# Kernel optimization log

Measured on AMD Instinct MI355X. Metric: run time of the kernel, lower is better.

The kernel has to match this reference:

```python
import jax, jax.numpy as jnp
import numpy as np

N_NODES = 50000
N_EDGES = 600000
D = 128
HIDDEN = 128
OUT = 1


def setup_inputs() -> dict:
    key = jax.random.key(0)
    ks = jax.random.split(key, 6)
    z = jax.random.normal(ks[0], (N_NODES, D), dtype=jnp.float32)
    e = jax.random.randint(ks[1], (2, N_EDGES), 0, N_NODES, dtype=jnp.int64)
    # Linear weights in [in, out] layout; scaled like torch default init
    W1 = jax.random.normal(ks[2], (2 * D, HIDDEN), dtype=jnp.float32) / np.sqrt(2 * D)
    b1 = jax.random.normal(ks[3], (HIDDEN,), dtype=jnp.float32) / np.sqrt(2 * D)
    W2 = jax.random.normal(ks[4], (HIDDEN, OUT), dtype=jnp.float32) / np.sqrt(HIDDEN)
    b2 = jax.random.normal(ks[5], (OUT,), dtype=jnp.float32) / np.sqrt(HIDDEN)
    return {"z": z, "e": e, "W1": W1, "b1": b1, "W2": W2, "b2": b2}


def reference(z, e, W1, b1, W2, b2):
    x_i = z[e[0]]                      # [E, D] gather source nodes
    x_j = z[e[1]]                      # [E, D] gather target nodes
    x = jnp.concatenate([x_i, x_j], axis=1)  # [E, 2D]
    h = jax.nn.relu(x @ W1 + b1)       # [E, HIDDEN]
    out = h @ W2 + b2                  # [E, OUT]
    return jax.nn.sigmoid(out).squeeze()  # [E]
```

## Files before the change

kernel.cpp:

```cpp
#include <hip/hip_runtime.h>


#define DD 128

typedef __attribute__((ext_vector_type(8))) short short8;
typedef __attribute__((ext_vector_type(4))) float floatx4;

static __device__ __forceinline__ unsigned short f2bf(float f) {
  unsigned int u = __builtin_bit_cast(unsigned int, f);
  u += 0x7fffu + ((u >> 16) & 1u);
  return (unsigned short)(u >> 16);
}
static __device__ __forceinline__ float bf2f(unsigned short u) {
  return __builtin_bit_cast(float, (unsigned int)u << 16);
}

__global__ __launch_bounds__(256) void wt_build(
    const float* __restrict__ W1, unsigned short* __restrict__ Wt) {
  const int g = blockIdx.x * 256 + threadIdx.x;
  const int c = g >> 5;
  const int kq = (g & 31) * 4;
  const float* src = (c < 128) ? (W1 + c) : (W1 + 128 * 128 + (c - 128));
  ushort4 o;
  o.x = f2bf(src[(size_t)(kq + 0) * 128]);
  o.y = f2bf(src[(size_t)(kq + 1) * 128]);
  o.z = f2bf(src[(size_t)(kq + 2) * 128]);
  o.w = f2bf(src[(size_t)(kq + 3) * 128]);
  *(ushort4*)&Wt[c * 128 + kq] = o;
}

__global__ __launch_bounds__(512, 4) void node_mfma(
    const float* __restrict__ z, const unsigned short* __restrict__ Wt,
    const float* __restrict__ b1, signed char* __restrict__ gqi,
    signed char* __restrict__ gqj, float* __restrict__ sci,
    float* __restrict__ scj, int n_nodes) {
  __shared__ __align__(16) unsigned short zb[64 * 136];
  const int tid = threadIdx.x;
  const int nb = blockIdx.x * 64;

#pragma unroll
  for (int i = 0; i < 4; ++i) {
    int q = tid + i * 512;
    int nl = q >> 5;
    int node = nb + nl; if (node >= n_nodes) node = n_nodes - 1;
    float4 v = ((const float4*)z)[(size_t)node * 32 + (q & 31)];
    ushort4 o;
    o.x = f2bf(v.x); o.y = f2bf(v.y); o.z = f2bf(v.z); o.w = f2bf(v.w);
    *(ushort4*)&zb[nl * 136 + (q & 31) * 4] = o;
  }

  const int w = tid >> 6, lane = tid & 63;
  const int l15 = lane & 15, quad = lane >> 4;

  short8 a[2][4];
#pragma unroll
  for (int tt = 0; tt < 2; ++tt) {
    const unsigned short* wrow =
        Wt + (size_t)((w * 2 + tt) * 16 + l15) * 128 + quad * 8;
#pragma unroll
    for (int s = 0; s < 4; ++s) a[tt][s] = *(const short8*)(wrow + s * 32);
  }

  floatx4 acc[2][4];
#pragma unroll
  for (int tt = 0; tt < 2; ++tt) {
    floatx4 bias = {0.f, 0.f, 0.f, 0.f};
    if (w < 4) {
      float4 b4 = *(const float4*)&b1[(w * 2 + tt) * 16 + quad * 4];
      bias[0] = b4.x; bias[1] = b4.y; bias[2] = b4.z; bias[3] = b4.w;
    }
#pragma unroll
    for (int nt = 0; nt < 4; ++nt) acc[tt][nt] = bias;
  }

  __syncthreads();

#pragma unroll
  for (int nt = 0; nt < 4; ++nt) {
    short8 bz[4];
#pragma unroll
    for (int s = 0; s < 4; ++s)
      bz[s] = *(const short8*)&zb[(nt * 16 + l15) * 136 + s * 32 + quad * 8];
#pragma unroll
    for (int tt = 0; tt < 2; ++tt)
#pragma unroll
      for (int s = 0; s < 4; ++s)
        acc[tt][nt] = __builtin_amdgcn_mfma_f32_16x16x32_bf16(
            a[tt][s], bz[s], acc[tt][nt], 0, 0, 0);
  }

  __syncthreads();
#pragma unroll
  for (int half = 0; half < 2; ++half) {
    if ((w >> 2) == half) {
      const int cbase = (w & 3) * 32;
#pragma unroll
      for (int nt = 0; nt < 4; ++nt) {
        const int row = (nt * 16 + l15) * 136;
#pragma unroll
        for (int tt = 0; tt < 2; ++tt) {
          const int c = cbase + tt * 16 + quad * 4;
          ushort4 o;
          o.x = f2bf(acc[tt][nt][0]); o.y = f2bf(acc[tt][nt][1]);
          o.z = f2bf(acc[tt][nt][2]); o.w = f2bf(acc[tt][nt][3]);
          *(ushort4*)&zb[row + c] = o;
        }
      }
    }
    __syncthreads();
    {
      const int nl = tid >> 3, p8 = tid & 7;
      const int node = nb + nl;
      const unsigned short* rowp = &zb[nl * 136 + p8 * 16];
      ushort4 u0 = *(const ushort4*)(rowp);
      ushort4 u1 = *(const ushort4*)(rowp + 4);
      ushort4 u2 = *(const ushort4*)(rowp + 8);
      ushort4 u3 = *(const ushort4*)(rowp + 12);
      float f[16];
      f[0] = bf2f(u0.x); f[1] = bf2f(u0.y); f[2] = bf2f(u0.z); f[3] = bf2f(u0.w);
      f[4] = bf2f(u1.x); f[5] = bf2f(u1.y); f[6] = bf2f(u1.z); f[7] = bf2f(u1.w);
      f[8] = bf2f(u2.x); f[9] = bf2f(u2.y); f[10] = bf2f(u2.z); f[11] = bf2f(u2.w);
      f[12] = bf2f(u3.x); f[13] = bf2f(u3.y); f[14] = bf2f(u3.z); f[15] = bf2f(u3.w);
      float am = 0.f;
#pragma unroll
      for (int k = 0; k < 16; ++k) am = fmaxf(am, fabsf(f[k]));
      am = fmaxf(am, __shfl_xor(am, 1));
      am = fmaxf(am, __shfl_xor(am, 2));
      am = fmaxf(am, __shfl_xor(am, 4));
      const float inv = (am > 0.f) ? 127.f / am : 0.f;
      unsigned int wd[4];
#pragma unroll
      for (int k2 = 0; k2 < 4; ++k2) {
        unsigned int v = 0;
#pragma unroll
        for (int b = 0; b < 4; ++b) {
          const int q = (int)rintf(f[k2 * 4 + b] * inv);
          v |= ((unsigned int)(q & 0xff)) << (8 * b);
        }
        wd[k2] = v;
      }
      if (node < n_nodes) {
        signed char* dq = half ? gqj : gqi;
        uint4 pk; pk.x = wd[0]; pk.y = wd[1]; pk.z = wd[2]; pk.w = wd[3];
        ((uint4*)(dq + (size_t)node * 128))[p8] = pk;
        if (p8 == 0) (half ? scj : sci)[node] = am * (1.f / 127.f);
      }
    }
    __syncthreads();
  }
}

__global__ __launch_bounds__(256) void edge_mlp_q(
    const int* __restrict__ e, const signed char* __restrict__ gqi,
    const signed char* __restrict__ gqj, const float* __restrict__ sci,
    const float* __restrict__ scj, const float* __restrict__ W2,
    const float* __restrict__ b2, float* __restrict__ out, int E) {
  const int p = threadIdx.x & 7;
  const float4* wv = (const float4*)W2;
  float4 W[4];
#pragma unroll
  for (int k = 0; k < 4; ++k) W[k] = wv[p * 4 + k];
  const float bias2 = b2[0];

  const int stride = gridDim.x * 32;
  for (int edge = blockIdx.x * 32 + (threadIdx.x >> 3); edge < E; edge += stride) {
    const int i = e[edge];
    const int j = e[E + edge];
    const float si = sci[i];
    const float sj = scj[j];
    const uint4 qa = ((const uint4*)(gqi + (size_t)i * 128))[p];
    const uint4 qb = ((const uint4*)(gqj + (size_t)j * 128))[p];
    const unsigned int ua[4] = {qa.x, qa.y, qa.z, qa.w};
    const unsigned int ub[4] = {qb.x, qb.y, qb.z, qb.w};
    float acc = 0.f;
#pragma unroll
    for (int k = 0; k < 4; ++k) {
      const float wk[4] = {W[k].x, W[k].y, W[k].z, W[k].w};
#pragma unroll
      for (int b = 0; b < 4; ++b) {
        const float af = (float)(int)(signed char)(ua[k] >> (8 * b));
        const float bf = (float)(int)(signed char)(ub[k] >> (8 * b));
        const float h = fmaf(si, af, sj * bf);
        acc = fmaf(fmaxf(h, 0.f), wk[b], acc);
      }
    }
    acc += __shfl_xor(acc, 1);
    acc += __shfl_xor(acc, 2);
    acc += __shfl_xor(acc, 4);
    if (p == 0) {
      out[edge] = 1.f / (1.f + __expf(-(acc + bias2)));
    }
  }
}

__global__ __launch_bounds__(256) void edge_direct(
    const int* __restrict__ e, const float* __restrict__ z,
    const float* __restrict__ W1, const float* __restrict__ b1,
    const float* __restrict__ W2, const float* __restrict__ b2,
    float* __restrict__ out, int E) {
  const int lane = threadIdx.x & 63;
  const int edge = (int)((blockIdx.x * 256u + threadIdx.x) >> 6);
  if (edge >= E) return;
  const int i = e[edge], j = e[E + edge];
  const float* zi = z + (size_t)i * 128;
  const float* zj = z + (size_t)j * 128;
  const int c0 = lane * 2;
  float h0 = b1[c0], h1 = b1[c0 + 1];
  for (int k = 0; k < 128; ++k) {
    float a = zi[k], b = zj[k];
    float2 wt = *(const float2*)&W1[(size_t)k * 128 + c0];
    float2 wb = *(const float2*)&W1[(size_t)(128 + k) * 128 + c0];
    h0 = fmaf(a, wt.x, h0); h1 = fmaf(a, wt.y, h1);
    h0 = fmaf(b, wb.x, h0); h1 = fmaf(b, wb.y, h1);
  }
  float s = fmaxf(h0, 0.f) * W2[c0] + fmaxf(h1, 0.f) * W2[c0 + 1];
#pragma unroll
  for (int off = 1; off < 64; off <<= 1) s += __shfl_xor(s, off);
  if (lane == 0) out[edge] = 1.f / (1.f + __expf(-(s + b2[0])));
}

extern "C" void kernel_launch(void* const* d_in, const int* in_sizes, int n_in,
                              void* d_out, int out_size, void* d_ws, size_t ws_size,
                              hipStream_t stream) {
  const float* z  = (const float*)d_in[0];
  const int*   e  = (const int*)d_in[1];
  const float* W1 = (const float*)d_in[2];
  const float* b1 = (const float*)d_in[3];
  const float* W2 = (const float*)d_in[4];
  const float* b2 = (const float*)d_in[5];
  float* out = (float*)d_out;
  const int n_nodes = in_sizes[0] / DD;
  const int E = in_sizes[1] / 2;

  const size_t gq_bytes = (size_t)n_nodes * DD;
  const size_t sc_bytes = (size_t)n_nodes * sizeof(float);
  const size_t wt_bytes = 256 * 128 * sizeof(unsigned short);
  const size_t need = 2 * gq_bytes + 2 * sc_bytes + wt_bytes;

  if (ws_size >= need && n_nodes > 0) {
    signed char* gqi = (signed char*)d_ws;
    signed char* gqj = gqi + gq_bytes;
    float* sci = (float*)((char*)d_ws + 2 * gq_bytes);
    float* scj = (float*)((char*)d_ws + 2 * gq_bytes + sc_bytes);
    unsigned short* Wt =
        (unsigned short*)((char*)d_ws + 2 * gq_bytes + 2 * sc_bytes);
    wt_build<<<32, 256, 0, stream>>>(W1, Wt);
    node_mfma<<<(n_nodes + 63) / 64, 512, 0, stream>>>(z, Wt, b1, gqi, gqj,
                                                       sci, scj, n_nodes);
    edge_mlp_q<<<2048, 256, 0, stream>>>(e, gqi, gqj, sci, scj, W2, b2, out, E);
  } else {
    edge_direct<<<(E + 3) / 4, 256, 0, stream>>>(e, z, W1, b1, W2, b2, out, E);
  }
}
```

Before: 114.7 us.

## Quantize node projections directly from MFMA registers with shared atomic max

The epilogue no longer stages bf16 accumulators in LDS in two serialized halves. Each wave now computes per-node absmax from its fp32 accumulators and combines them through LDS atomicMax. It then quantizes to int8 in registers and writes the packed words to a padded LDS buffer, which both halves store out in one pass. This removes the extra bf16 rounding, several barriers and the per-half serialization, at the cost of additional LDS and shared atomics. Quantization is now based on fp32 rather than bf16-rounded values, so results may differ slightly.

Measured after the change: 113.9 us. Within noise of the previous version (-0.7%).

```diff
diff --git a/kernel.cpp b/kernel.cpp
--- a/kernel.cpp
+++ b/kernel.cpp
@@ -10,9 +10,6 @@
   unsigned int u = __builtin_bit_cast(unsigned int, f);
   u += 0x7fffu + ((u >> 16) & 1u);
   return (unsigned short)(u >> 16);
-}
-static __device__ __forceinline__ float bf2f(unsigned short u) {
-  return __builtin_bit_cast(float, (unsigned int)u << 16);
 }
 
 __global__ __launch_bounds__(256) void wt_build(
@@ -35,8 +32,12 @@
     signed char* __restrict__ gqj, float* __restrict__ sci,
     float* __restrict__ scj, int n_nodes) {
   __shared__ __align__(16) unsigned short zb[64 * 136];
+  __shared__ unsigned int ep[2 * 64 * 33];
+  __shared__ unsigned int smax[2][64];
   const int tid = threadIdx.x;
   const int nb = blockIdx.x * 64;
+
+  if (tid < 128) smax[tid >> 6][tid & 63] = 0u;
 
 #pragma unroll
   for (int i = 0; i < 4; ++i) {
@@ -89,64 +90,64 @@
             a[tt][s], bz[s], acc[tt][nt], 0, 0, 0);
   }
 
+  const int half = w >> 2;
+  const int cbase = (w & 3) * 32;
+
+#pragma unroll
+  for (int nt = 0; nt < 4; ++nt) {
+    float m = 0.f;
+#pragma unroll
+    for (int tt = 0; tt < 2; ++tt)
+#pragma unroll
+      for (int r = 0; r < 4; ++r) m = fmaxf(m, fabsf(acc[tt][nt][r]));
+    m = fmaxf(m, __shfl_xor(m, 16));
+    m = fmaxf(m, __shfl_xor(m, 32));
+    if (lane < 16)
+      atomicMax(&smax[half][nt * 16 + lane], __float_as_uint(m));
+  }
   __syncthreads();
-#pragma unroll
-  for (int half = 0; half < 2; ++half) {
-    if ((w >> 2) == half) {
-      const int cbase = (w & 3) * 32;
-#pragma unroll
-      for (int nt = 0; nt < 4; ++nt) {
-        const int row = (nt * 16 + l15) * 136;
-#pragma unroll
-        for (int tt = 0; tt < 2; ++tt) {
-          const int c = cbase + tt * 16 + quad * 4;
-          ushort4 o;
-          o.x = f2bf(acc[tt][nt][0]); o.y = f2bf(acc[tt][nt][1]);
-          o.z = f2bf(acc[tt][nt][2]); o.w = f2bf(acc[tt][nt][3]);
-          *(ushort4*)&zb[row + c] = o;
-        }
+
+#pragma unroll
+  for (int nt = 0; nt < 4; ++nt) {
+    const int node_l = nt * 16 + l15;
+    const float am = __uint_as_float(smax[half][node_l]);
+    const float inv = (am > 0.f) ? 127.f / am : 0.f;
+#pragma unroll
+    for (int tt = 0; tt < 2; ++tt) {
+      unsigned int v = 0;
+#pragma unroll
+      for (int r = 0; r < 4; ++r) {
+        const int q = (int)rintf(acc[tt][nt][r] * inv);
+        v |= ((unsigned int)(q & 0xff)) << (8 * r);
       }
-    }
-    __syncthreads();
-    {
-      const int nl = tid >> 3, p8 = tid & 7;
-      const int node = nb + nl;
-      const unsigned short* rowp = &zb[nl * 136 + p8 * 16];
-      ushort4 u0 = *(const ushort4*)(rowp);
-      ushort4 u1 = *(const ushort4*)(rowp + 4);
-      ushort4 u2 = *(const ushort4*)(rowp + 8);
-      ushort4 u3 = *(const ushort4*)(rowp + 12);
-      float f[16];
-      f[0] = bf2f(u0.x); f[1] = bf2f(u0.y); f[2] = bf2f(u0.z); f[3] = bf2f(u0.w);
-      f[4] = bf2f(u1.x); f[5] = bf2f(u1.y); f[6] = bf2f(u1.z); f[7] = bf2f(u1.w);
-      f[8] = bf2f(u2.x); f[9] = bf2f(u2.y); f[10] = bf2f(u2.z); f[11] = bf2f(u2.w);
-      f[12] = bf2f(u3.x); f[13] = bf2f(u3.y); f[14] = bf2f(u3.z); f[15] = bf2f(u3.w);
-      float am = 0.f;
-#pragma unroll
-      for (int k = 0; k < 16; ++k) am = fmaxf(am, fabsf(f[k]));
-      am = fmaxf(am, __shfl_xor(am, 1));
-      am = fmaxf(am, __shfl_xor(am, 2));
-      am = fmaxf(am, __shfl_xor(am, 4));
-      const float inv = (am > 0.f) ? 127.f / am : 0.f;
-      unsigned int wd[4];
-#pragma unroll
-      for (int k2 = 0; k2 < 4; ++k2) {
-        unsigned int v = 0;
-#pragma unroll
-        for (int b = 0; b < 4; ++b) {
-          const int q = (int)rintf(f[k2 * 4 + b] * inv);
-          v |= ((unsigned int)(q & 0xff)) << (8 * b);
-        }
-        wd[k2] = v;
+      ep[half * 2112 + node_l * 33 + ((cbase + tt * 16 + quad * 4) >> 2)] = v;
+    }
+  }
+  __syncthreads();
+
+  {
+    const int hh = tid >> 8;
+    const int sub = tid & 255;
+    const int nl = sub >> 2;
+    const int c32 = (sub & 3) * 32;
+    const int node = nb + nl;
+    const unsigned int* rp = &ep[hh * 2112 + nl * 33 + (c32 >> 2)];
+    uint4 o0, o1;
+    o0.x = rp[0]; o0.y = rp[1]; o0.z = rp[2]; o0.w = rp[3];
+    o1.x = rp[4]; o1.y = rp[5]; o1.z = rp[6]; o1.w = rp[7];
+    if (node < n_nodes) {
+      signed char* dq = hh ? gqj : gqi;
+      uint4* gp = (uint4*)(dq + (size_t)node * 128 + c32);
+      gp[0] = o0; gp[1] = o1;
+    }
+    if (tid < 128) {
+      const int h2 = tid >> 6, n2 = tid & 63;
+      const int node2 = nb + n2;
+      if (node2 < n_nodes) {
+        const float amv = __uint_as_float(smax[h2][n2]);
+        (h2 ? scj : sci)[node2] = amv * (1.f / 127.f);
       }
-      if (node < n_nodes) {
-        signed char* dq = half ? gqj : gqi;
-        uint4 pk; pk.x = wd[0]; pk.y = wd[1]; pk.z = wd[2]; pk.w = wd[3];
-        ((uint4*)(dq + (size_t)node * 128))[p8] = pk;
-        if (p8 == 0) (half ? scj : sci)[node] = am * (1.f / 127.f);
-      }
-    }
-    __syncthreads();
+    }
   }
 }
 
```
